# Kernel tuning notes

Measured on AMD Instinct MI355X. Metric: run time of the kernel, lower is better.

Reference implementation:

```python
import math
import jax, jax.numpy as jnp
import numpy as np

BATCH = 64
N_SAMPLES = 131072
SAMPLE_RATE = 48000
CUTOFF = 1000.0
RESONANCE = 0.7


def setup_inputs() -> dict:
    key = jax.random.key(0)
    audio = jax.random.normal(key, (BATCH, N_SAMPLES), dtype=jnp.float32)
    g = jnp.asarray(math.tan(math.pi / SAMPLE_RATE * CUTOFF), dtype=jnp.float32)
    twoR = jnp.asarray(1.0 / RESONANCE, dtype=jnp.float32)
    mix = jnp.array([0.0, 1.0, 0.0], dtype=jnp.float32)  # lowpass: mix of (bp, lp, hp)
    return {"audio": audio, "g": g, "twoR": twoR, "mix": mix}


def reference(audio, g, twoR, mix):
    # audio: [batch, n_samples]; g, twoR: scalars; mix: [3]
    x = audio.T  # time-first: [n_samples, batch]
    one = jnp.ones_like(g)
    T = 1.0 / (1.0 + g * (g + twoR))
    # H = T * [[1, -g], [g, twoR*g + 1]]  (constant 2x2 transition matrix)
    H = T * jnp.stack([jnp.stack([one, -g]), jnp.stack([g, twoR * g + one])])
    gHB = g * T * jnp.stack([one, g])  # [2] input gain vector

    def step(state, x_t):
        # state: [batch, 2]; x_t: [batch]
        y = gHB[None, :] * x_t[:, None] + state @ H.T  # [batch, 2]
        return 2.0 * y - state, y

    init = jnp.zeros((x.shape[1], 2), dtype=audio.dtype)
    _, Y = jax.lax.scan(step, init, x)  # Y: [n_samples, batch, 2]

    y_bp, y_lp = Y[..., 0], Y[..., 1]
    y_hp = x - twoR * y_bp - y_lp
    y_mixed = twoR * mix[0] * y_bp + mix[1] * y_lp + mix[2] * y_hp
    return y_mixed.T  # [batch, n_samples]
```

## Files before the change

### kernel.cpp

```cpp
#include <hip/hip_runtime.h>


#define BATCH 64
#define NS    131072
#define CLEN  128
#define WARM  128
#define CPB   64
#define TT    32
#define NTILE ((CLEN + WARM) / TT)
#define ETILE (WARM / TT)
#define LROW  (CPB + 1)

__global__ __launch_bounds__(64) void svf_fused(
        const float* __restrict__ audio,
        const float* __restrict__ gp,
        const float* __restrict__ twoRp,
        const float* __restrict__ mixp,
        float* __restrict__ out) {
    __shared__ float lds[TT * LROW];

    const int lane = threadIdx.x;
    const int bpr  = (NS / CLEN) / CPB;
    const int b    = blockIdx.x / bpr;
    const int chunk0 = (blockIdx.x % bpr) * CPB;

    const float* X = audio + (size_t)b * NS;
    float*       O = out   + (size_t)b * NS;

    const float g = gp[0], twoR = twoRp[0];
    const float T   = 1.0f / (1.0f + g * (g + twoR));
    const float h00 = T, h01 = -T * g, h10 = T * g, h11 = T * (twoR * g + 1.0f);
    const float a00 = 2.f * h00 - 1.f, a01 = 2.f * h01;
    const float a10 = 2.f * h10,       a11 = 2.f * h11 - 1.f;
    const float b0 = 2.f * g * T, b1 = 2.f * g * T * g;
    const float gb0 = g * T, gb1 = g * T * g;
    const float m0 = mixp[0], m1 = mixp[1], m2 = mixp[2];
    const float cbp = twoR * (m0 - m2), clp = m1 - m2;
    const float p  = m2 + cbp * gb0 + clp * gb1;
    const float q0 = cbp * h00 + clp * h10;
    const float q1 = cbp * h01 + clp * h11;

    const int base = chunk0 * CLEN - WARM;

    float4 pf[8];
#pragma unroll
    for (int i = 0; i < 8; ++i) {
        int j4 = i * 64 + lane;
        int c  = j4 >> 3, t4 = j4 & 7;
        int f  = base + c * CLEN + t4 * 4;
        pf[i] = (f >= 0) ? *reinterpret_cast<const float4*>(X + f)
                         : make_float4(0.f, 0.f, 0.f, 0.f);
    }

    float s0 = 0.f, s1 = 0.f;

    for (int k = 0; k < NTILE; ++k) {
        __syncthreads();
#pragma unroll
        for (int i = 0; i < 8; ++i) {
            int j4 = i * 64 + lane;
            int c  = j4 >> 3, t4 = j4 & 7;
            float* lp = &lds[(t4 * 4) * LROW + c];
            lp[0 * LROW] = pf[i].x; lp[1 * LROW] = pf[i].y;
            lp[2 * LROW] = pf[i].z; lp[3 * LROW] = pf[i].w;
        }
        __syncthreads();

        if (k + 1 < NTILE) {
#pragma unroll
            for (int i = 0; i < 8; ++i) {
                int j4 = i * 64 + lane;
                int c  = j4 >> 3, t4 = j4 & 7;
                int f  = base + c * CLEN + (k + 1) * TT + t4 * 4;
                pf[i] = (f >= 0) ? *reinterpret_cast<const float4*>(X + f)
                                 : make_float4(0.f, 0.f, 0.f, 0.f);
            }
        }

        if (k < ETILE) {
#pragma unroll
            for (int t = 0; t < TT; ++t) {
                float x  = lds[t * LROW + lane];
                float n0 = fmaf(a00, s0, fmaf(a01, s1, b0 * x));
                float n1 = fmaf(a10, s0, fmaf(a11, s1, b1 * x));
                s0 = n0; s1 = n1;
            }
        } else {
#pragma unroll
            for (int t = 0; t < TT; ++t) {
                float x  = lds[t * LROW + lane];
                float o  = fmaf(p, x, fmaf(q0, s0, q1 * s1));
                float n0 = fmaf(a00, s0, fmaf(a01, s1, b0 * x));
                float n1 = fmaf(a10, s0, fmaf(a11, s1, b1 * x));
                s0 = n0; s1 = n1;
                lds[t * LROW + lane] = o;
            }
            __syncthreads();
#pragma unroll
            for (int i = 0; i < 8; ++i) {
                int j4 = i * 64 + lane;
                int c  = j4 >> 3, t4 = j4 & 7;
                const float* lp = &lds[(t4 * 4) * LROW + c];
                float4 o4 = make_float4(lp[0], lp[1 * LROW],
                                        lp[2 * LROW], lp[3 * LROW]);
                int fo = (chunk0 + c) * CLEN + (k - ETILE) * TT + t4 * 4;
                *reinterpret_cast<float4*>(O + fo) = o4;
            }
        }
    }
}

extern "C" void kernel_launch(void* const* d_in, const int* in_sizes, int n_in,
                              void* d_out, int out_size, void* d_ws, size_t ws_size,
                              hipStream_t stream) {
    const float* audio = (const float*)d_in[0];
    const float* gp    = (const float*)d_in[1];
    const float* twoRp = (const float*)d_in[2];
    const float* mixp  = (const float*)d_in[3];
    float* out = (float*)d_out;

    const int blocks = BATCH * ((NS / CLEN) / CPB);
    svf_fused<<<blocks, CPB, 0, stream>>>(audio, gp, twoRp, mixp, out);
}
```

Before: 91.93 us.

## Stage whole block window in LDS and reuse neighbor chunks as warmup

Chunk length drops to 64 and each block loads 66 consecutive chunks into LDS in one pass. Each lane warms up on the two preceding chunks, which the neighbouring lanes also use as their own data, instead of re-reading a separate 128-sample warmup from global memory. The tiled, double-buffered time loop and its per-tile syncs are gone, and outputs are written back with nontemporal stores. This cuts redundant global reads and syncs, but the block count doubles, the LDS footprint grows, and the single load phase no longer overlaps loads with compute.

```diff
diff --git a/kernel.cpp b/kernel.cpp
--- a/kernel.cpp
+++ b/kernel.cpp
@@ -3,26 +3,27 @@
 
 #define BATCH 64
 #define NS    131072
-#define CLEN  128
-#define WARM  128
-#define CPB   64
-#define TT    32
-#define NTILE ((CLEN + WARM) / TT)
-#define ETILE (WARM / TT)
-#define LROW  (CPB + 1)
+#define CLEN  64
+#define NCH   (NS / CLEN)
+#define BPR   (NCH / 64)
+#define NCOL  66
+#define CST   66
+#define NF4   (NCOL * CLEN / 4)
+#define LD_IT ((NF4 + 63) / 64)
 
-__global__ __launch_bounds__(64) void svf_fused(
+typedef float vfloat4 __attribute__((ext_vector_type(4)));
+
+__global__ __launch_bounds__(64) void svf_lds(
         const float* __restrict__ audio,
         const float* __restrict__ gp,
         const float* __restrict__ twoRp,
         const float* __restrict__ mixp,
         float* __restrict__ out) {
-    __shared__ float lds[TT * LROW];
+    __shared__ float lds[NCOL * CST];
 
-    const int lane = threadIdx.x;
-    const int bpr  = (NS / CLEN) / CPB;
-    const int b    = blockIdx.x / bpr;
-    const int chunk0 = (blockIdx.x % bpr) * CPB;
+    const int lane   = threadIdx.x;
+    const int b      = blockIdx.x / BPR;
+    const int chunk0 = (blockIdx.x % BPR) * 64;
 
     const float* X = audio + (size_t)b * NS;
     float*       O = out   + (size_t)b * NS;
@@ -40,73 +41,70 @@
     const float q0 = cbp * h00 + clp * h10;
     const float q1 = cbp * h01 + clp * h11;
 
-    const int base = chunk0 * CLEN - WARM;
+    const int base_f = (chunk0 - 2) * CLEN;
 
-    float4 pf[8];
+    vfloat4 pf[LD_IT];
 #pragma unroll
-    for (int i = 0; i < 8; ++i) {
-        int j4 = i * 64 + lane;
-        int c  = j4 >> 3, t4 = j4 & 7;
-        int f  = base + c * CLEN + t4 * 4;
-        pf[i] = (f >= 0) ? *reinterpret_cast<const float4*>(X + f)
-                         : make_float4(0.f, 0.f, 0.f, 0.f);
+    for (int i = 0; i < LD_IT; ++i) {
+        const int j4 = i * 64 + lane;
+        const int f  = base_f + (j4 >> 4) * CLEN + (j4 & 15) * 4;
+        pf[i] = (j4 < NF4 && f >= 0)
+                    ? *reinterpret_cast<const vfloat4*>(X + f)
+                    : (vfloat4)(0.f);
     }
+#pragma unroll
+    for (int i = 0; i < LD_IT; ++i) {
+        const int j4 = i * 64 + lane;
+        if (j4 < NF4) {
+            const int col = j4 >> 4, t4 = j4 & 15;
+            float2* lp = reinterpret_cast<float2*>(&lds[col * CST + t4 * 4]);
+            lp[0] = make_float2(pf[i].x, pf[i].y);
+            lp[1] = make_float2(pf[i].z, pf[i].w);
+        }
+    }
+    __syncthreads();
 
     float s0 = 0.f, s1 = 0.f;
+    const int cbase = lane * CST;
+#pragma unroll
+    for (int t = 0; t < CLEN; ++t) {
+        const float x  = lds[cbase + t];
+        const float n0 = fmaf(a00, s0, fmaf(a01, s1, b0 * x));
+        const float n1 = fmaf(a10, s0, fmaf(a11, s1, b1 * x));
+        s0 = n0; s1 = n1;
+    }
+#pragma unroll
+    for (int t = 0; t < CLEN; ++t) {
+        const float x  = lds[cbase + CST + t];
+        const float n0 = fmaf(a00, s0, fmaf(a01, s1, b0 * x));
+        const float n1 = fmaf(a10, s0, fmaf(a11, s1, b1 * x));
+        s0 = n0; s1 = n1;
+    }
+    __syncthreads();
 
-    for (int k = 0; k < NTILE; ++k) {
-        __syncthreads();
+    const int ebase = cbase + 2 * CST;
 #pragma unroll
-        for (int i = 0; i < 8; ++i) {
-            int j4 = i * 64 + lane;
-            int c  = j4 >> 3, t4 = j4 & 7;
-            float* lp = &lds[(t4 * 4) * LROW + c];
-            lp[0 * LROW] = pf[i].x; lp[1 * LROW] = pf[i].y;
-            lp[2 * LROW] = pf[i].z; lp[3 * LROW] = pf[i].w;
-        }
-        __syncthreads();
+    for (int t = 0; t < CLEN; ++t) {
+        const float x  = lds[ebase + t];
+        const float o  = fmaf(p, x, fmaf(q0, s0, q1 * s1));
+        const float n0 = fmaf(a00, s0, fmaf(a01, s1, b0 * x));
+        const float n1 = fmaf(a10, s0, fmaf(a11, s1, b1 * x));
+        s0 = n0; s1 = n1;
+        lds[ebase + t] = o;
+    }
+    __syncthreads();
 
-        if (k + 1 < NTILE) {
 #pragma unroll
-            for (int i = 0; i < 8; ++i) {
-                int j4 = i * 64 + lane;
-                int c  = j4 >> 3, t4 = j4 & 7;
-                int f  = base + c * CLEN + (k + 1) * TT + t4 * 4;
-                pf[i] = (f >= 0) ? *reinterpret_cast<const float4*>(X + f)
-                                 : make_float4(0.f, 0.f, 0.f, 0.f);
-            }
-        }
-
-        if (k < ETILE) {
-#pragma unroll
-            for (int t = 0; t < TT; ++t) {
-                float x  = lds[t * LROW + lane];
-                float n0 = fmaf(a00, s0, fmaf(a01, s1, b0 * x));
-                float n1 = fmaf(a10, s0, fmaf(a11, s1, b1 * x));
-                s0 = n0; s1 = n1;
-            }
-        } else {
-#pragma unroll
-            for (int t = 0; t < TT; ++t) {
-                float x  = lds[t * LROW + lane];
-                float o  = fmaf(p, x, fmaf(q0, s0, q1 * s1));
-                float n0 = fmaf(a00, s0, fmaf(a01, s1, b0 * x));
-                float n1 = fmaf(a10, s0, fmaf(a11, s1, b1 * x));
-                s0 = n0; s1 = n1;
-                lds[t * LROW + lane] = o;
-            }
-            __syncthreads();
-#pragma unroll
-            for (int i = 0; i < 8; ++i) {
-                int j4 = i * 64 + lane;
-                int c  = j4 >> 3, t4 = j4 & 7;
-                const float* lp = &lds[(t4 * 4) * LROW + c];
-                float4 o4 = make_float4(lp[0], lp[1 * LROW],
-                                        lp[2 * LROW], lp[3 * LROW]);
-                int fo = (chunk0 + c) * CLEN + (k - ETILE) * TT + t4 * 4;
-                *reinterpret_cast<float4*>(O + fo) = o4;
-            }
-        }
+    for (int i = 0; i < 16; ++i) {
+        const int j4  = i * 64 + lane;
+        const int c   = j4 >> 4, t4 = j4 & 15;
+        const float2* lp =
+            reinterpret_cast<const float2*>(&lds[(c + 2) * CST + t4 * 4]);
+        const float2 lo = lp[0], hi = lp[1];
+        vfloat4 o4;
+        o4.x = lo.x; o4.y = lo.y; o4.z = hi.x; o4.w = hi.y;
+        const int fo = (chunk0 + c) * CLEN + t4 * 4;
+        __builtin_nontemporal_store(o4, reinterpret_cast<vfloat4*>(O + fo));
     }
 }
 
@@ -119,6 +117,6 @@
     const float* mixp  = (const float*)d_in[3];
     float* out = (float*)d_out;
 
-    const int blocks = BATCH * ((NS / CLEN) / CPB);
-    svf_fused<<<blocks, CPB, 0, stream>>>(audio, gp, twoRp, mixp, out);
+    const int blocks = BATCH * BPR;
+    svf_lds<<<blocks, 64, 0, stream>>>(audio, gp, twoRp, mixp, out);
 }
```

Measured after the change: 88.13 us. 4.1% less time.
